# Kernel optimization log

Measured on AMD Instinct MI355X. Metric: run time of the kernel, lower is better.

## Reference

```python
import jax, jax.numpy as jnp
import numpy as np

N_HEADS = 6

def setup_inputs() -> dict:
    key = jax.random.key(0)
    ks = jax.random.split(key, 5)
    B, N, E = 4, 2048, 96
    scale = 0.02
    return {
        "x": jax.random.normal(ks[0], (B, N, E), dtype=jnp.float32),
        "Wqkv": jax.random.normal(ks[1], (E, 3 * E), dtype=jnp.float32) * scale,
        "bqkv": jax.random.normal(ks[2], (3 * E,), dtype=jnp.float32) * scale,
        "Wff": jax.random.normal(ks[3], (E, E), dtype=jnp.float32) * scale,
        "bff": jax.random.normal(ks[4], (E,), dtype=jnp.float32) * scale,
    }

def reference(x, Wqkv, bqkv, Wff, bff):
    B, N, E = x.shape
    H = N_HEADS
    D = E // H  # head_dim = 16
    qkv = x @ Wqkv + bqkv  # [B, N, 3E]
    q, k, v = jnp.split(qkv, 3, axis=-1)
    # [B, N, E] -> [B, H, N, D]
    q = q.reshape(B, N, H, D).transpose(0, 2, 1, 3)
    k = k.reshape(B, N, H, D).transpose(0, 2, 1, 3)
    v = v.reshape(B, N, H, D).transpose(0, 2, 1, 3)
    # unnormalized (no softmax) scaled dot-product attention
    attn = jnp.einsum("bhnd,bhmd->bhnm", q, k) * (D ** -0.5)  # [B, H, N, N]
    y = jnp.einsum("bhnm,bhmd->bhnd", attn, v)                # [B, H, N, D]
    y = y.transpose(0, 2, 1, 3).reshape(B, N, E)
    return y @ Wff + bff
```

## Files before the change

### kernel.cpp

```cpp
#include <hip/hip_runtime.h>

#define BB 4
#define NTOK 2048
#define E 96
#define NH 6
#define E3 288
#define MSZ 1536
#define SCALE 0.25f

typedef __attribute__((ext_vector_type(8))) short bf16x8;
typedef __attribute__((ext_vector_type(4))) float f32x4;

__device__ __forceinline__ short f2bf(float f) {
    unsigned u = __float_as_uint(f);
    u += 0x7fff + ((u >> 16) & 1);
    return (short)(u >> 16);
}

__global__ __launch_bounds__(256) void k_kv(const float* __restrict__ x,
                                            const float* __restrict__ Wqkv,
                                            const float* __restrict__ bqkv,
                                            float* __restrict__ Mg) {
    const int b = blockIdx.x >> 6, tile = blockIdx.x & 63;
    const int n0 = tile * 32;
    const int t = threadIdx.x;
    __shared__ short xb[32 * 104];
    __shared__ short wkvT[192 * 104];
    __shared__ short kvn[192 * 40];

    {
        const float4* src = (const float4*)(x + ((size_t)b * NTOK + n0) * E);
        for (int f = t; f < 768; f += 256) {
            float4 v = src[f];
            int r = f / 24, c4 = (f % 24) * 4;
            short4 s = { f2bf(v.x), f2bf(v.y), f2bf(v.z), f2bf(v.w) };
            *(short4*)&xb[r * 104 + c4] = s;
        }
    }
    {
        for (int f = t; f < 2304; f += 256) {
            int ep = f / 48, cq = (f % 48) * 4;
            const float4 a = *(const float4*)(Wqkv + (size_t)(2 * ep) * E3 + E + cq);
            const float4 c = *(const float4*)(Wqkv + (size_t)(2 * ep + 1) * E3 + E + cq);
            *(short2*)&wkvT[(cq + 0) * 104 + 2 * ep] = make_short2(f2bf(a.x), f2bf(c.x));
            *(short2*)&wkvT[(cq + 1) * 104 + 2 * ep] = make_short2(f2bf(a.y), f2bf(c.y));
            *(short2*)&wkvT[(cq + 2) * 104 + 2 * ep] = make_short2(f2bf(a.z), f2bf(c.z));
            *(short2*)&wkvT[(cq + 3) * 104 + 2 * ep] = make_short2(f2bf(a.w), f2bf(c.w));
        }
    }
    __syncthreads();

    const int w = t >> 6, lane = t & 63;
    const int rhalf = w & 1, chalf = w >> 1;
    const int lr = lane & 15, kg = lane >> 4;

    {
        f32x4 acc[6];
#pragma unroll
        for (int j = 0; j < 6; j++) acc[j] = (f32x4){0.f, 0.f, 0.f, 0.f};
#pragma unroll
        for (int ks = 0; ks < 3; ks++) {
            const bf16x8 af = *(const bf16x8*)&xb[(rhalf * 16 + lr) * 104 + ks * 32 + kg * 8];
#pragma unroll
            for (int j = 0; j < 6; j++) {
                const bf16x8 bf = *(const bf16x8*)&wkvT[(chalf * 96 + j * 16 + lr) * 104 + ks * 32 + kg * 8];
                acc[j] = __builtin_amdgcn_mfma_f32_16x16x32_bf16(af, bf, acc[j], 0, 0, 0);
            }
        }
        const int nr = rhalf * 16 + kg * 4;
#pragma unroll
        for (int j = 0; j < 6; j++) {
            const int cg = chalf * 96 + j * 16 + lr;
            const float bias = bqkv[E + cg];
            short4 s = { f2bf(acc[j][0] + bias), f2bf(acc[j][1] + bias),
                         f2bf(acc[j][2] + bias), f2bf(acc[j][3] + bias) };
            *(short4*)&kvn[cg * 40 + nr] = s;
        }
    }
    __syncthreads();

    {
        for (int h = w; h < NH; h += 4) {
            const bf16x8 ka = *(const bf16x8*)&kvn[(h * 16 + lr) * 40 + kg * 8];
            const bf16x8 vb = *(const bf16x8*)&kvn[(96 + h * 16 + lr) * 40 + kg * 8];
            f32x4 mc = (f32x4){0.f, 0.f, 0.f, 0.f};
            mc = __builtin_amdgcn_mfma_f32_16x16x32_bf16(ka, vb, mc, 0, 0, 0);
            float* base = &Mg[b * MSZ + h * 256];
            const int d2 = lr, d1b = kg * 4;
            unsafeAtomicAdd(base + (d1b + 0) * 16 + d2, mc[0]);
            unsafeAtomicAdd(base + (d1b + 1) * 16 + d2, mc[1]);
            unsafeAtomicAdd(base + (d1b + 2) * 16 + d2, mc[2]);
            unsafeAtomicAdd(base + (d1b + 3) * 16 + d2, mc[3]);
        }
    }
}

__global__ __launch_bounds__(256) void k_out(const float* __restrict__ x,
                                             const float* __restrict__ Wqkv,
                                             const float* __restrict__ bqkv,
                                             const float* __restrict__ Wff,
                                             const float* __restrict__ bff,
                                             const float* __restrict__ Mg,
                                             float* __restrict__ out) {
    const int b = blockIdx.x >> 6, tile = blockIdx.x & 63;
    const int n0 = tile * 32;
    const int t = threadIdx.x;
    __shared__ short xb[32 * 104];
    __shared__ short wT[96 * 104];
    __shared__ short t2b[32 * 104];
    __shared__ float qs[32 * 100];
    __shared__ float Ms2[NH * 320];

    {
        const float4* src = (const float4*)(x + ((size_t)b * NTOK + n0) * E);
        for (int f = t; f < 768; f += 256) {
            float4 v = src[f];
            int r = f / 24, c4 = (f % 24) * 4;
            short4 s = { f2bf(v.x), f2bf(v.y), f2bf(v.z), f2bf(v.w) };
            *(short4*)&xb[r * 104 + c4] = s;
        }
    }
    {
        for (int f = t; f < 1152; f += 256) {
            int ep = f / 24, cq = (f % 24) * 4;
            const float4 a = *(const float4*)(Wqkv + (size_t)(2 * ep) * E3 + cq);
            const float4 c = *(const float4*)(Wqkv + (size_t)(2 * ep + 1) * E3 + cq);
            *(short2*)&wT[(cq + 0) * 104 + 2 * ep] = make_short2(f2bf(a.x), f2bf(c.x));
            *(short2*)&wT[(cq + 1) * 104 + 2 * ep] = make_short2(f2bf(a.y), f2bf(c.y));
            *(short2*)&wT[(cq + 2) * 104 + 2 * ep] = make_short2(f2bf(a.z), f2bf(c.z));
            *(short2*)&wT[(cq + 3) * 104 + 2 * ep] = make_short2(f2bf(a.w), f2bf(c.w));
        }
    }
    {
#pragma unroll
        for (int i = 0; i < 6; i++) {
            const int o = t + i * 256;
            const int h = o >> 8, d1 = (o >> 4) & 15, d2 = o & 15;
            Ms2[h * 320 + d2 * 20 + d1] = SCALE * Mg[b * MSZ + o];
        }
    }
    __syncthreads();

    const int w = t >> 6, lane = t & 63;
    const int rhalf = w & 1, chalf = w >> 1;
    const int lr = lane & 15, kg = lane >> 4;
    const int nr = rhalf * 16 + kg * 4;

    {
        f32x4 acc[3];
#pragma unroll
        for (int j = 0; j < 3; j++) acc[j] = (f32x4){0.f, 0.f, 0.f, 0.f};
#pragma unroll
        for (int ks = 0; ks < 3; ks++) {
            const bf16x8 af = *(const bf16x8*)&xb[(rhalf * 16 + lr) * 104 + ks * 32 + kg * 8];
#pragma unroll
            for (int j = 0; j < 3; j++) {
                const bf16x8 bf = *(const bf16x8*)&wT[(chalf * 48 + j * 16 + lr) * 104 + ks * 32 + kg * 8];
                acc[j] = __builtin_amdgcn_mfma_f32_16x16x32_bf16(af, bf, acc[j], 0, 0, 0);
            }
        }
#pragma unroll
        for (int j = 0; j < 3; j++) {
            const int col = chalf * 48 + j * 16 + lr;
            const float bq = bqkv[col];
            qs[(nr + 0) * 100 + col] = acc[j][0] + bq;
            qs[(nr + 1) * 100 + col] = acc[j][1] + bq;
            qs[(nr + 2) * 100 + col] = acc[j][2] + bq;
            qs[(nr + 3) * 100 + col] = acc[j][3] + bq;
        }
    }
    __syncthreads();

    {
        for (int f = t; f < 1152; f += 256) {
            int ep = f / 24, cq = (f % 24) * 4;
            const float4 a = *(const float4*)(Wff + (size_t)(2 * ep) * E + cq);
            const float4 c = *(const float4*)(Wff + (size_t)(2 * ep + 1) * E + cq);
            *(short2*)&wT[(cq + 0) * 104 + 2 * ep] = make_short2(f2bf(a.x), f2bf(c.x));
            *(short2*)&wT[(cq + 1) * 104 + 2 * ep] = make_short2(f2bf(a.y), f2bf(c.y));
            *(short2*)&wT[(cq + 2) * 104 + 2 * ep] = make_short2(f2bf(a.z), f2bf(c.z));
            *(short2*)&wT[(cq + 3) * 104 + 2 * ep] = make_short2(f2bf(a.w), f2bf(c.w));
        }
        const int r = t >> 3, tc0 = (t & 7) * 12;
        const int h0 = tc0 >> 4, h1 = (tc0 + 11) >> 4;
        float4 qa[4], qb[4];
#pragma unroll
        for (int u = 0; u < 4; u++) {
            qa[u] = *(const float4*)&qs[r * 100 + h0 * 16 + u * 4];
            qb[u] = *(const float4*)&qs[r * 100 + h1 * 16 + u * 4];
        }
        float t2v[12];
#pragma unroll
        for (int j = 0; j < 12; j++) {
            const int c = tc0 + j, h = c >> 4, d2 = c & 15;
            const float4* mrow = (const float4*)&Ms2[h * 320 + d2 * 20];
            float v = 0.f;
#pragma unroll
            for (int u = 0; u < 4; u++) {
                const float4 qv = (h == h0) ? qa[u] : qb[u];
                const float4 mf = mrow[u];
                v += qv.x * mf.x + qv.y * mf.y + qv.z * mf.z + qv.w * mf.w;
            }
            t2v[j] = v;
        }
#pragma unroll
        for (int q3 = 0; q3 < 3; q3++) {
            short4 s = { f2bf(t2v[q3 * 4]), f2bf(t2v[q3 * 4 + 1]),
                         f2bf(t2v[q3 * 4 + 2]), f2bf(t2v[q3 * 4 + 3]) };
            *(short4*)&t2b[r * 104 + tc0 + q3 * 4] = s;
        }
    }
    __syncthreads();

    {
        f32x4 acc[3];
#pragma unroll
        for (int j = 0; j < 3; j++) acc[j] = (f32x4){0.f, 0.f, 0.f, 0.f};
#pragma unroll
        for (int ks = 0; ks < 3; ks++) {
            const bf16x8 af = *(const bf16x8*)&t2b[(rhalf * 16 + lr) * 104 + ks * 32 + kg * 8];
#pragma unroll
            for (int j = 0; j < 3; j++) {
                const bf16x8 bf = *(const bf16x8*)&wT[(chalf * 48 + j * 16 + lr) * 104 + ks * 32 + kg * 8];
                acc[j] = __builtin_amdgcn_mfma_f32_16x16x32_bf16(af, bf, acc[j], 0, 0, 0);
            }
        }
        float* obase = out + ((size_t)b * NTOK + n0 + nr) * E;
#pragma unroll
        for (int j = 0; j < 3; j++) {
            const int col = chalf * 48 + j * 16 + lr;
            const float bv = bff[col];
            obase[0 * E + col] = acc[j][0] + bv;
            obase[1 * E + col] = acc[j][1] + bv;
            obase[2 * E + col] = acc[j][2] + bv;
            obase[3 * E + col] = acc[j][3] + bv;
        }
    }
}

extern "C" void kernel_launch(void* const* d_in, const int* in_sizes, int n_in,
                              void* d_out, int out_size, void* d_ws, size_t ws_size,
                              hipStream_t stream) {
    const float* x    = (const float*)d_in[0];
    const float* Wqkv = (const float*)d_in[1];
    const float* bqkv = (const float*)d_in[2];
    const float* Wff  = (const float*)d_in[3];
    const float* bff  = (const float*)d_in[4];
    float* out = (float*)d_out;
    float* Mg  = (float*)d_ws;

    hipMemsetAsync(Mg, 0, (size_t)BB * MSZ * sizeof(float), stream);
    k_kv<<<BB * 64, 256, 0, stream>>>(x, Wqkv, bqkv, Mg);
    k_out<<<BB * 64, 256, 0, stream>>>(x, Wqkv, bqkv, Wff, bff, Mg, out);
}
```

Before: 22.77 us.

## Replace atomic K^T V reduction with per-tile bf16 partials reduced in output kernel

Each k_kv block now writes its per-head 16x16 K^T V partial as bf16 into its own slot instead of atomically adding fp32 into a shared buffer. This removes the memset launch and the atomic contention. k_out blocks reduce the 64 partials per batch themselves, redundantly in every block, and block indices are remapped with an XCD-aware swizzle. In exchange, the partials lose precision from bf16 rounding, and every output block repeats the same 64-slot reduction read.

```diff
diff --git a/kernel.cpp b/kernel.cpp
--- a/kernel.cpp
+++ b/kernel.cpp
@@ -1,4 +1,5 @@
 #include <hip/hip_runtime.h>
+#include <hip/hip_bf16.h>
 
 #define BB 4
 #define NTOK 2048
@@ -12,16 +13,16 @@
 typedef __attribute__((ext_vector_type(4))) float f32x4;
 
 __device__ __forceinline__ short f2bf(float f) {
-    unsigned u = __float_as_uint(f);
-    u += 0x7fff + ((u >> 16) & 1);
-    return (short)(u >> 16);
+    __hip_bfloat16 h = __float2bfloat16(f);
+    return __builtin_bit_cast(short, h);
 }
 
 __global__ __launch_bounds__(256) void k_kv(const float* __restrict__ x,
                                             const float* __restrict__ Wqkv,
                                             const float* __restrict__ bqkv,
-                                            float* __restrict__ Mg) {
-    const int b = blockIdx.x >> 6, tile = blockIdx.x & 63;
+                                            short* __restrict__ Mp) {
+    const int L = ((blockIdx.x & 7) << 5) | (blockIdx.x >> 3);
+    const int b = L >> 6, tile = L & 63;
     const int n0 = tile * 32;
     const int t = threadIdx.x;
     __shared__ short xb[32 * 104];
@@ -80,17 +81,14 @@
     __syncthreads();
 
     {
+        short* mpt = Mp + (size_t)L * MSZ;
         for (int h = w; h < NH; h += 4) {
             const bf16x8 ka = *(const bf16x8*)&kvn[(h * 16 + lr) * 40 + kg * 8];
             const bf16x8 vb = *(const bf16x8*)&kvn[(96 + h * 16 + lr) * 40 + kg * 8];
             f32x4 mc = (f32x4){0.f, 0.f, 0.f, 0.f};
             mc = __builtin_amdgcn_mfma_f32_16x16x32_bf16(ka, vb, mc, 0, 0, 0);
-            float* base = &Mg[b * MSZ + h * 256];
-            const int d2 = lr, d1b = kg * 4;
-            unsafeAtomicAdd(base + (d1b + 0) * 16 + d2, mc[0]);
-            unsafeAtomicAdd(base + (d1b + 1) * 16 + d2, mc[1]);
-            unsafeAtomicAdd(base + (d1b + 2) * 16 + d2, mc[2]);
-            unsafeAtomicAdd(base + (d1b + 3) * 16 + d2, mc[3]);
+            short4 s = { f2bf(mc[0]), f2bf(mc[1]), f2bf(mc[2]), f2bf(mc[3]) };
+            *(short4*)&mpt[h * 256 + lane * 4] = s;
         }
     }
 }
@@ -100,9 +98,10 @@
                                              const float* __restrict__ bqkv,
                                              const float* __restrict__ Wff,
                                              const float* __restrict__ bff,
-                                             const float* __restrict__ Mg,
+                                             const short* __restrict__ Mp,
                                              float* __restrict__ out) {
-    const int b = blockIdx.x >> 6, tile = blockIdx.x & 63;
+    const int L = ((blockIdx.x & 7) << 5) | (blockIdx.x >> 3);
+    const int b = L >> 6, tile = L & 63;
     const int n0 = tile * 32;
     const int t = threadIdx.x;
     __shared__ short xb[32 * 104];
@@ -132,11 +131,24 @@
         }
     }
     {
-#pragma unroll
-        for (int i = 0; i < 6; i++) {
-            const int o = t + i * 256;
-            const int h = o >> 8, d1 = (o >> 4) & 15, d2 = o & 15;
-            Ms2[h * 320 + d2 * 20 + d1] = SCALE * Mg[b * MSZ + o];
+        if (t < 192) {
+            float racc[8];
+#pragma unroll
+            for (int j = 0; j < 8; j++) racc[j] = 0.f;
+            const short* mpb = Mp + (size_t)b * 64 * MSZ + t * 8;
+#pragma unroll 8
+            for (int tl = 0; tl < 64; ++tl) {
+                const bf16x8 v = *(const bf16x8*)(mpb + (size_t)tl * MSZ);
+#pragma unroll
+                for (int j = 0; j < 8; j++)
+                    racc[j] += __uint_as_float(((unsigned)(unsigned short)v[j]) << 16);
+            }
+#pragma unroll
+            for (int j = 0; j < 8; j++) {
+                const int o = t * 8 + j;
+                const int h = o >> 8, kg = (o >> 6) & 3, lr = (o >> 2) & 15, i = o & 3;
+                Ms2[h * 320 + lr * 20 + kg * 4 + i] = SCALE * racc[j];
+            }
         }
     }
     __syncthreads();
@@ -247,9 +259,8 @@
     const float* Wff  = (const float*)d_in[3];
     const float* bff  = (const float*)d_in[4];
     float* out = (float*)d_out;
-    float* Mg  = (float*)d_ws;
-
-    hipMemsetAsync(Mg, 0, (size_t)BB * MSZ * sizeof(float), stream);
-    k_kv<<<BB * 64, 256, 0, stream>>>(x, Wqkv, bqkv, Mg);
-    k_out<<<BB * 64, 256, 0, stream>>>(x, Wqkv, bqkv, Wff, bff, Mg, out);
-}
+    short* Mp  = (short*)d_ws;
+
+    k_kv<<<BB * 64, 256, 0, stream>>>(x, Wqkv, bqkv, Mp);
+    k_out<<<BB * 64, 256, 0, stream>>>(x, Wqkv, bqkv, Wff, bff, Mp, out);
+}
```

Result: faster. 19.70 us (-13.5%).

## Fuse KV and output kernels into one launch with per-batch grid barrier

Applied to the files above, without the earlier changes.

Merges the two kernels into a single persistent-style kernel. Each block computes its K^T V partial, accumulates it atomically, bumps a per-batch counter, computes Q, prefetches Wff, then spin-waits until all 64 blocks of its batch have contributed before applying M. This removes one kernel launch and the reload of x. It relies on all 256 blocks being co-resident to avoid deadlock, and it also swaps the manual bf16 rounding for the library conversion.

```diff
diff --git a/kernel.cpp b/kernel.cpp
--- a/kernel.cpp
+++ b/kernel.cpp
@@ -1,4 +1,5 @@
 #include <hip/hip_runtime.h>
+#include <hip/hip_bf16.h>
 
 #define BB 4
 #define NTOK 2048
@@ -12,21 +13,30 @@
 typedef __attribute__((ext_vector_type(4))) float f32x4;
 
 __device__ __forceinline__ short f2bf(float f) {
-    unsigned u = __float_as_uint(f);
-    u += 0x7fff + ((u >> 16) & 1);
-    return (short)(u >> 16);
+    __hip_bfloat16 h = __float2bfloat16(f);
+    return __builtin_bit_cast(short, h);
 }
 
-__global__ __launch_bounds__(256) void k_kv(const float* __restrict__ x,
-                                            const float* __restrict__ Wqkv,
-                                            const float* __restrict__ bqkv,
-                                            float* __restrict__ Mg) {
-    const int b = blockIdx.x >> 6, tile = blockIdx.x & 63;
+__global__ __launch_bounds__(256) void k_all(const float* __restrict__ x,
+                                             const float* __restrict__ Wqkv,
+                                             const float* __restrict__ bqkv,
+                                             const float* __restrict__ Wff,
+                                             const float* __restrict__ bff,
+                                             float* __restrict__ Mg,
+                                             unsigned int* __restrict__ cnt,
+                                             float* __restrict__ out) {
+    const int L = ((blockIdx.x & 7) << 5) | (blockIdx.x >> 3);
+    const int b = L >> 6, tile = L & 63;
     const int n0 = tile * 32;
     const int t = threadIdx.x;
+
     __shared__ short xb[32 * 104];
     __shared__ short wkvT[192 * 104];
     __shared__ short kvn[192 * 40];
+    __shared__ short wT[96 * 104];
+    __shared__ float qs[32 * 100];
+    __shared__ float Ms2[NH * 320];
+    __shared__ short t2b[32 * 104];
 
     {
         const float4* src = (const float4*)(x + ((size_t)b * NTOK + n0) * E);
@@ -48,78 +58,6 @@
             *(short2*)&wkvT[(cq + 3) * 104 + 2 * ep] = make_short2(f2bf(a.w), f2bf(c.w));
         }
     }
-    __syncthreads();
-
-    const int w = t >> 6, lane = t & 63;
-    const int rhalf = w & 1, chalf = w >> 1;
-    const int lr = lane & 15, kg = lane >> 4;
-
-    {
-        f32x4 acc[6];
-#pragma unroll
-        for (int j = 0; j < 6; j++) acc[j] = (f32x4){0.f, 0.f, 0.f, 0.f};
-#pragma unroll
-        for (int ks = 0; ks < 3; ks++) {
-            const bf16x8 af = *(const bf16x8*)&xb[(rhalf * 16 + lr) * 104 + ks * 32 + kg * 8];
-#pragma unroll
-            for (int j = 0; j < 6; j++) {
-                const bf16x8 bf = *(const bf16x8*)&wkvT[(chalf * 96 + j * 16 + lr) * 104 + ks * 32 + kg * 8];
-                acc[j] = __builtin_amdgcn_mfma_f32_16x16x32_bf16(af, bf, acc[j], 0, 0, 0);
-            }
-        }
-        const int nr = rhalf * 16 + kg * 4;
-#pragma unroll
-        for (int j = 0; j < 6; j++) {
-            const int cg = chalf * 96 + j * 16 + lr;
-            const float bias = bqkv[E + cg];
-            short4 s = { f2bf(acc[j][0] + bias), f2bf(acc[j][1] + bias),
-                         f2bf(acc[j][2] + bias), f2bf(acc[j][3] + bias) };
-            *(short4*)&kvn[cg * 40 + nr] = s;
-        }
-    }
-    __syncthreads();
-
-    {
-        for (int h = w; h < NH; h += 4) {
-            const bf16x8 ka = *(const bf16x8*)&kvn[(h * 16 + lr) * 40 + kg * 8];
-            const bf16x8 vb = *(const bf16x8*)&kvn[(96 + h * 16 + lr) * 40 + kg * 8];
-            f32x4 mc = (f32x4){0.f, 0.f, 0.f, 0.f};
-            mc = __builtin_amdgcn_mfma_f32_16x16x32_bf16(ka, vb, mc, 0, 0, 0);
-            float* base = &Mg[b * MSZ + h * 256];
-            const int d2 = lr, d1b = kg * 4;
-            unsafeAtomicAdd(base + (d1b + 0) * 16 + d2, mc[0]);
-            unsafeAtomicAdd(base + (d1b + 1) * 16 + d2, mc[1]);
-            unsafeAtomicAdd(base + (d1b + 2) * 16 + d2, mc[2]);
-            unsafeAtomicAdd(base + (d1b + 3) * 16 + d2, mc[3]);
-        }
-    }
-}
-
-__global__ __launch_bounds__(256) void k_out(const float* __restrict__ x,
-                                             const float* __restrict__ Wqkv,
-                                             const float* __restrict__ bqkv,
-                                             const float* __restrict__ Wff,
-                                             const float* __restrict__ bff,
-                                             const float* __restrict__ Mg,
-                                             float* __restrict__ out) {
-    const int b = blockIdx.x >> 6, tile = blockIdx.x & 63;
-    const int n0 = tile * 32;
-    const int t = threadIdx.x;
-    __shared__ short xb[32 * 104];
-    __shared__ short wT[96 * 104];
-    __shared__ short t2b[32 * 104];
-    __shared__ float qs[32 * 100];
-    __shared__ float Ms2[NH * 320];
-
-    {
-        const float4* src = (const float4*)(x + ((size_t)b * NTOK + n0) * E);
-        for (int f = t; f < 768; f += 256) {
-            float4 v = src[f];
-            int r = f / 24, c4 = (f % 24) * 4;
-            short4 s = { f2bf(v.x), f2bf(v.y), f2bf(v.z), f2bf(v.w) };
-            *(short4*)&xb[r * 104 + c4] = s;
-        }
-    }
     {
         for (int f = t; f < 1152; f += 256) {
             int ep = f / 24, cq = (f % 24) * 4;
@@ -131,22 +69,57 @@
             *(short2*)&wT[(cq + 3) * 104 + 2 * ep] = make_short2(f2bf(a.w), f2bf(c.w));
         }
     }
-    {
-#pragma unroll
-        for (int i = 0; i < 6; i++) {
-            const int o = t + i * 256;
-            const int h = o >> 8, d1 = (o >> 4) & 15, d2 = o & 15;
-            Ms2[h * 320 + d2 * 20 + d1] = SCALE * Mg[b * MSZ + o];
-        }
-    }
     __syncthreads();
 
     const int w = t >> 6, lane = t & 63;
-    const int rhalf = w & 1, chalf = w >> 1;
     const int lr = lane & 15, kg = lane >> 4;
+    const int rhalf = w & 1;
     const int nr = rhalf * 16 + kg * 4;
 
     {
+        const int chalf = w >> 1;
+        f32x4 acc[6];
+#pragma unroll
+        for (int j = 0; j < 6; j++) acc[j] = (f32x4){0.f, 0.f, 0.f, 0.f};
+#pragma unroll
+        for (int ks = 0; ks < 3; ks++) {
+            const bf16x8 af = *(const bf16x8*)&xb[(rhalf * 16 + lr) * 104 + ks * 32 + kg * 8];
+#pragma unroll
+            for (int j = 0; j < 6; j++) {
+                const bf16x8 bf = *(const bf16x8*)&wkvT[(chalf * 96 + j * 16 + lr) * 104 + ks * 32 + kg * 8];
+                acc[j] = __builtin_amdgcn_mfma_f32_16x16x32_bf16(af, bf, acc[j], 0, 0, 0);
+            }
+        }
+#pragma unroll
+        for (int j = 0; j < 6; j++) {
+            const int cg = chalf * 96 + j * 16 + lr;
+            const float bias = bqkv[E + cg];
+            short4 s = { f2bf(acc[j][0] + bias), f2bf(acc[j][1] + bias),
+                         f2bf(acc[j][2] + bias), f2bf(acc[j][3] + bias) };
+            *(short4*)&kvn[cg * 40 + nr] = s;
+        }
+    }
+    __syncthreads();
+
+    {
+        for (int h = w; h < NH; h += 4) {
+            const bf16x8 ka = *(const bf16x8*)&kvn[(h * 16 + lr) * 40 + kg * 8];
+            const bf16x8 vb = *(const bf16x8*)&kvn[(96 + h * 16 + lr) * 40 + kg * 8];
+            f32x4 mc = (f32x4){0.f, 0.f, 0.f, 0.f};
+            mc = __builtin_amdgcn_mfma_f32_16x16x32_bf16(ka, vb, mc, 0, 0, 0);
+            float* base = &Mg[b * MSZ + h * 256];
+            unsafeAtomicAdd(base + (kg * 4 + 0) * 16 + lr, mc[0]);
+            unsafeAtomicAdd(base + (kg * 4 + 1) * 16 + lr, mc[1]);
+            unsafeAtomicAdd(base + (kg * 4 + 2) * 16 + lr, mc[2]);
+            unsafeAtomicAdd(base + (kg * 4 + 3) * 16 + lr, mc[3]);
+        }
+    }
+    __threadfence();
+    __syncthreads();
+    if (t == 0) atomicAdd(&cnt[b], 1u);
+
+    {
+        const int chalf = w >> 1;
         f32x4 acc[3];
 #pragma unroll
         for (int j = 0; j < 3; j++) acc[j] = (f32x4){0.f, 0.f, 0.f, 0.f};
@@ -181,6 +154,25 @@
             *(short2*)&wT[(cq + 2) * 104 + 2 * ep] = make_short2(f2bf(a.z), f2bf(c.z));
             *(short2*)&wT[(cq + 3) * 104 + 2 * ep] = make_short2(f2bf(a.w), f2bf(c.w));
         }
+    }
+    if (t == 0) {
+        while (__hip_atomic_load(&cnt[b], __ATOMIC_RELAXED, __HIP_MEMORY_SCOPE_AGENT) < 64u)
+            __builtin_amdgcn_s_sleep(8);
+    }
+    __syncthreads();
+
+    {
+#pragma unroll
+        for (int i = 0; i < 6; i++) {
+            const int o = t + i * 256;
+            const int h = o >> 8, d1 = (o >> 4) & 15, d2 = o & 15;
+            Ms2[h * 320 + d2 * 20 + d1] =
+                SCALE * __hip_atomic_load(&Mg[b * MSZ + o], __ATOMIC_RELAXED, __HIP_MEMORY_SCOPE_AGENT);
+        }
+    }
+    __syncthreads();
+
+    {
         const int r = t >> 3, tc0 = (t & 7) * 12;
         const int h0 = tc0 >> 4, h1 = (tc0 + 11) >> 4;
         float4 qa[4], qb[4];
@@ -213,6 +205,7 @@
     __syncthreads();
 
     {
+        const int chalf = w >> 1;
         f32x4 acc[3];
 #pragma unroll
         for (int j = 0; j < 3; j++) acc[j] = (f32x4){0.f, 0.f, 0.f, 0.f};
@@ -248,8 +241,8 @@
     const float* bff  = (const float*)d_in[4];
     float* out = (float*)d_out;
     float* Mg  = (float*)d_ws;
-
-    hipMemsetAsync(Mg, 0, (size_t)BB * MSZ * sizeof(float), stream);
-    k_kv<<<BB * 64, 256, 0, stream>>>(x, Wqkv, bqkv, Mg);
-    k_out<<<BB * 64, 256, 0, stream>>>(x, Wqkv, bqkv, Wff, bff, Mg, out);
+    unsigned int* cnt = (unsigned int*)(Mg + BB * MSZ);
+
+    hipMemsetAsync(d_ws, 0, (size_t)BB * MSZ * sizeof(float) + BB * sizeof(unsigned int), stream);
+    k_all<<<BB * 64, 256, 0, stream>>>(x, Wqkv, bqkv, Wff, bff, Mg, cnt, out);
 }
```

Result: slower. 34.55 us (+51.7%).
